# Kernel optimization log

Hardware: AMD Instinct MI355X
Metric: run time of the kernel (lower is better)

## Reference

```python
import jax, jax.numpy as jnp
import numpy as np

B, NPG, F, H, DEG = 2048, 50, 64, 2, 8  # graphs, nodes/graph, feat dim, heads, avg degree
N = B * NPG
NEG_SLOPE_ATTN = 0.2   # DGL GATConv default leaky slope
NEG_SLOPE_ACT = 0.1    # module's LeakyReLU


def setup_inputs() -> dict:
    key = jax.random.key(0)
    ks = jax.random.split(key, 24)
    node_feats = jax.random.normal(ks[0], (N, F), dtype=jnp.float32)
    # within-graph random edges + self loops (avoids zero in-degree)
    E = N * DEG
    base = jnp.repeat(jnp.arange(B, dtype=jnp.int32) * NPG, NPG * DEG)
    src = base + jax.random.randint(ks[1], (E,), 0, NPG, dtype=jnp.int32)
    dst = base + jax.random.randint(ks[2], (E,), 0, NPG, dtype=jnp.int32)
    loops = jnp.arange(N, dtype=jnp.int32)
    src = jnp.concatenate([src, loops])
    dst = jnp.concatenate([dst, loops])
    s = 0.1
    params = dict(
        W0=jax.random.normal(ks[3], (F, H * F)) * s,
        al0=jax.random.normal(ks[4], (H, F)) * s,
        ar0=jax.random.normal(ks[5], (H, F)) * s,
        resW0=jax.random.normal(ks[6], (F, H * F)) * s,
        g0=jnp.ones((H * F,)), b0=jnp.zeros((H * F,)),
        W1=jax.random.normal(ks[7], (H * F, H * F)) * s,
        al1=jax.random.normal(ks[8], (H, F)) * s,
        ar1=jax.random.normal(ks[9], (H, F)) * s,
        g1=jnp.ones((H * F,)), b1=jnp.zeros((H * F,)),
        W2=jax.random.normal(ks[10], (H * F, H * F)) * s,
        al2=jax.random.normal(ks[11], (H, F)) * s,
        ar2=jax.random.normal(ks[12], (H, F)) * s,
        g2=jnp.ones((H * F,)), b2=jnp.zeros((H * F,)),
    )
    return {"node_feats": node_feats, **params, "src": src, "dst": dst}


def _gat(h, src, dst, W, al, ar, resW):
    """DGL GATConv (bias=False, residual=True, no activation). resW=None -> identity residual."""
    feat = (h @ W).reshape(N, H, F)                      # [N,H,F]
    el = jnp.sum(feat * al, -1)                          # [N,H]
    er = jnp.sum(feat * ar, -1)
    e = jax.nn.leaky_relu(el[src] + er[dst], NEG_SLOPE_ATTN)  # [E,H]
    m = jax.ops.segment_max(e, dst, num_segments=N)
    ex = jnp.exp(e - m[dst])
    denom = jax.ops.segment_sum(ex, dst, num_segments=N)
    a = ex / denom[dst]                                  # edge softmax per dst node
    rst = jax.ops.segment_sum(a[:, :, None] * feat[src], dst, num_segments=N)
    res = (h @ resW) if resW is not None else h
    return rst + res.reshape(N, H, F)


def _norm(x, g, b):
    mu = jnp.mean(x, -1, keepdims=True)
    v = jnp.mean((x - mu) ** 2, -1, keepdims=True)
    return (x - mu) / jnp.sqrt(v + 1e-5) * g + b


def reference(node_feats, W0, al0, ar0, resW0, g0, b0,
              W1, al1, ar1, g1, b1, W2, al2, ar2, g2, b2, src, dst):
    graph_ids = jnp.arange(N) // NPG
    layers = [(W0, al0, ar0, resW0, g0, b0),
              (W1, al1, ar1, None, g1, b1),
              (W2, al2, ar2, None, g2, b2)]
    h = node_feats
    embeddings = []
    for (W, al, ar, resW, g, b) in layers:
        h = _gat(h, src, dst, W, al, ar, resW).reshape(N, H * F)  # flatten(1)
        h = _norm(h, g, b)
        h = jax.nn.leaky_relu(h, NEG_SLOPE_ACT)
        per_node = h.reshape(N, H, F).mean(1)                     # mean over heads
        emb = jax.ops.segment_sum(per_node, graph_ids, num_segments=B) / NPG  # mean_nodes
        embeddings.append(emb)
    out = jnp.concatenate(embeddings, axis=-1)                    # JK 'cat' -> [B, 3F]
    return jax.nn.leaky_relu(out, NEG_SLOPE_ACT)
```

## Files before the change

kernel.cpp:

```cpp
#include <hip/hip_runtime.h>

#define NPG    50
#define HF     128
#define FDIM   64
#define NGRAPH 2048
#define EPG    400
#define SP     72
#define HB     136
#define CNTW   16

typedef __attribute__((ext_vector_type(8))) short bf16x8;
typedef __attribute__((ext_vector_type(4))) float floatx4;
typedef __bf16 bfv2 __attribute__((ext_vector_type(2)));

__device__ __forceinline__ float leaky(float x, float s) { return x >= 0.f ? x : x * s; }

__device__ __forceinline__ unsigned short f2bf(float f) {
    __bf16 b = (__bf16)f;
    unsigned short u;
    __builtin_memcpy(&u, &b, 2);
    return u;
}
__device__ __forceinline__ unsigned f2bfpk(float a, float b) {
    bfv2 v;
    v[0] = (__bf16)a;
    v[1] = (__bf16)b;
    unsigned u;
    __builtin_memcpy(&u, &v, 4);
    return u;
}
__device__ __forceinline__ float bf2f(unsigned short h) {
    return __uint_as_float(((unsigned)h) << 16);
}
__device__ __forceinline__ int fkey(float f) { int b = __float_as_int(f); return b >= 0 ? b : b ^ 0x7fffffff; }
__device__ __forceinline__ float funkey(int k) { return __int_as_float(k >= 0 ? k : k ^ 0x7fffffff); }

template <int CTRL>
__device__ __forceinline__ float dpp_addx(float x) {
    int yi = __builtin_amdgcn_update_dpp(0, __float_as_int(x), CTRL, 0xf, 0xf, true);
    return x + __int_as_float(yi);
}
__device__ __forceinline__ float row16_sum(float x) {
    x = dpp_addx<0xB1>(x);
    x = dpp_addx<0x4E>(x);
    x = dpp_addx<0x141>(x);
    x = dpp_addx<0x140>(x);
    return x;
}


__global__ void prep_w(const float* __restrict__ W0, const float* __restrict__ rW0,
                       const float* __restrict__ W1, const float* __restrict__ W2,
                       const float* __restrict__ al0, const float* __restrict__ ar0,
                       const float* __restrict__ al1, const float* __restrict__ ar1,
                       const float* __restrict__ al2, const float* __restrict__ ar2,
                       unsigned short* __restrict__ wt0, unsigned short* __restrict__ wt1,
                       unsigned short* __restrict__ wt2) {
    if (blockIdx.x >= 64) {
        int gid = (blockIdx.x - 64) * 256 + threadIdx.x;
        if (gid < 1024) {
            int la = gid >> 6, k = gid & 63;
            unsigned short o = 0;
            if (la < 8) {
                const float* a = (la < 4) ? al0 : ar0;
                int h = (la >> 1) & 1;
                float v = 0.f;
                for (int f = 0; f < 64; ++f) v += W0[k * 128 + h * 64 + f] * a[h * 64 + f];
                __bf16 hi = (__bf16)v;
                if (la & 1) o = f2bf(v - (float)hi);
                else __builtin_memcpy(&o, &hi, 2);
            }
            wt0[(256 + la) * 64 + k] = o;
        } else {
            int q = gid - 1024;
            int l = q >> 11;
            int la = (q >> 7) & 15, kp = q & 127;
            int ktrue = (kp & 64) + ((kp & 3) * 16) + ((kp & 63) >> 2);
            const float* W = l ? W2 : W1;
            unsigned short o = 0;
            if (la < 8) {
                const float* a = l ? ((la < 4) ? al2 : ar2) : ((la < 4) ? al1 : ar1);
                int h = (la >> 1) & 1;
                float v = 0.f;
                for (int f = 0; f < 64; ++f) v += W[ktrue * 128 + h * 64 + f] * a[h * 64 + f];
                __bf16 hi = (__bf16)v;
                if (la & 1) o = f2bf(v - (float)hi);
                else __builtin_memcpy(&o, &hi, 2);
            }
            (l ? wt2 : wt1)[(128 + la) * 128 + kp] = o;
        }
        return;
    }
    int i = blockIdx.x * 256 + threadIdx.x;
    if (i < 256 * 64) {
        int n = i >> 6, k = i & 63;
        float v = (n < 128) ? W0[k * 128 + n] : rW0[k * 128 + (n - 128)];
        wt0[i] = f2bf(v);
    }
    if (i < 128 * 128) {
        int n = i >> 7, kp = i & 127;
        int ktrue = (kp & 64) + ((kp & 3) * 16) + ((kp & 63) >> 2);
        wt1[i] = f2bf(W1[ktrue * 128 + n]);
        wt2[i] = f2bf(W2[ktrue * 128 + n]);
    }
}

template <int K, bool RESW>
__device__ __forceinline__ void gat_layer(
    const float* __restrict__ xrow,
    const unsigned short* __restrict__ Wt,
    const float* __restrict__ gp, const float* __restrict__ bp,
    float* __restrict__ out, int layer, int g, int t,
    unsigned short* featT, unsigned short* hbuf, int* cnt,
    float* el_s, float* er_s, int* elmax_i,
    float* lnp, float* lnq, float* psum4, float* gbL)
{
    const int w = t >> 6, lane = t & 63, quad = lane >> 4, l16 = lane & 15;
    constexpr int KS = K / 32;
    constexpr int ATTN_ROW = RESW ? 256 : 128;
    const int mt = w & 3;
    int mrow = mt * 16 + l16;
    if (mrow >= NPG) mrow = NPG - 1;
    const floatx4 zf = {0.f, 0.f, 0.f, 0.f};

    if (t < HF) {
        int p = (t & 64) + ((t & 15) * 4) + ((t >> 4) & 3);
        gbL[p] = gp[t];
        gbL[HF + p] = bp[t];
    }

    bf16x8 afr[KS];
    if constexpr (RESW) {
        const float* hrow = xrow + (size_t)mrow * 64;
#pragma unroll
        for (int ks = 0; ks < KS; ++ks) {
            int k0 = ks * 32 + quad * 8;
            float4 p0 = *(const float4*)(hrow + k0);
            float4 p1 = *(const float4*)(hrow + k0 + 4);
            unsigned au[4] = {f2bfpk(p0.x, p0.y), f2bfpk(p0.z, p0.w),
                              f2bfpk(p1.x, p1.y), f2bfpk(p1.z, p1.w)};
            __builtin_memcpy(&afr[ks], au, 16);
        }
    } else {
#pragma unroll
        for (int ks = 0; ks < KS; ++ks)
            afr[ks] = *(const bf16x8*)&hbuf[mrow * HB + ks * 32 + quad * 8];
    }

    if constexpr (RESW) {
#pragma unroll 1
        for (int half = 0; half < 2; ++half) {
            const int nb = (w >> 2) * 8 + half * 4;
            floatx4 acc[4];
#pragma unroll
            for (int nt = 0; nt < 4; ++nt) acc[nt] = zf;
#pragma unroll
            for (int nt = 0; nt < 4; ++nt) {
                const unsigned short* wrow = Wt + (size_t)((nb + nt) * 16 + l16) * K;
#pragma unroll
                for (int ks = 0; ks < KS; ++ks) {
                    bf16x8 b = *(const bf16x8*)(wrow + ks * 32 + quad * 8);
                    acc[nt] = __builtin_amdgcn_mfma_f32_16x16x32_bf16(afr[ks], b, acc[nt], 0, 0, 0);
                }
            }
#pragma unroll
            for (int nt = 0; nt < 4; ++nt) {
                int n = (nb + nt) * 16 + l16;
                if (n < HF) {
                    uint2 pk = {f2bfpk(acc[nt][0], acc[nt][1]),
                                f2bfpk(acc[nt][2], acc[nt][3])};
                    *(uint2*)&featT[n * SP + mt * 16 + quad * 4] = pk;
                } else {
                    int c = n - HF;
                    int spos = (c & 64) + ((c & 15) * 4) + ((c >> 4) & 3);
#pragma unroll
                    for (int r = 0; r < 4; ++r) {
                        int dr = mt * 16 + quad * 4 + r;
                        if (dr < NPG) hbuf[dr * HB + spos] = f2bf(acc[nt][r]);
                    }
                }
            }
        }
    } else {
        const int ntbase = (w >> 2) * 4;
        floatx4 acc[4];
#pragma unroll
        for (int nt = 0; nt < 4; ++nt) acc[nt] = zf;
#pragma unroll
        for (int nt = 0; nt < 4; ++nt) {
            const unsigned short* wrow = Wt + (size_t)((ntbase + nt) * 16 + l16) * K;
#pragma unroll
            for (int ks = 0; ks < KS; ++ks) {
                bf16x8 b = *(const bf16x8*)(wrow + ks * 32 + quad * 8);
                acc[nt] = __builtin_amdgcn_mfma_f32_16x16x32_bf16(afr[ks], b, acc[nt], 0, 0, 0);
            }
        }
#pragma unroll
        for (int nt = 0; nt < 4; ++nt) {
            int n = (ntbase + nt) * 16 + l16;
            uint2 pk = {f2bfpk(acc[nt][0], acc[nt][1]),
                        f2bfpk(acc[nt][2], acc[nt][3])};
            *(uint2*)&featT[n * SP + mt * 16 + quad * 4] = pk;
        }
    }

    if (w < 4) {
        floatx4 ae = zf;
        const unsigned short* wrow = Wt + (size_t)(ATTN_ROW + l16) * K;
#pragma unroll
        for (int ks = 0; ks < KS; ++ks) {
            bf16x8 b = *(const bf16x8*)(wrow + ks * 32 + quad * 8);
            ae = __builtin_amdgcn_mfma_f32_16x16x32_bf16(afr[ks], b, ae, 0, 0, 0);
        }
#pragma unroll
        for (int r = 0; r < 4; ++r) {
            float v = dpp_addx<0xB1>(ae[r]);
            if ((l16 & 1) == 0 && l16 < 8) {
                int row = mt * 16 + quad * 4 + r;
                int hd2 = (l16 >> 1) & 1;
                if (l16 < 4) {
                    el_s[hd2 * 64 + row] = v;
                    atomicMax(&elmax_i[hd2], fkey(v));
                } else {
                    er_s[hd2 * 64 + row] = v;
                }
            }
        }
    }
    __syncthreads();

    const int hd = w >> 2, amt = w & 3;
    const int d = amt * 16 + l16;

    const float erd = er_s[hd * 64 + d];
    const float md = leaky(funkey(elmax_i[hd]) + erd, 0.2f);
    const int dcl = d < NPG ? d : NPG - 1;
    const int* crow = &cnt[dcl * CNTW];

    bf16x8 ap[2];
    float rowsum = 0.f;
#pragma unroll
    for (int ks = 0; ks < 2; ++ks) {
        float4 ev0 = *(const float4*)&el_s[hd * 64 + ks * 32 + quad * 8];
        float4 ev1 = *(const float4*)&el_s[hd * 64 + ks * 32 + quad * 8 + 4];
        const float ev[8] = {ev0.x, ev0.y, ev0.z, ev0.w, ev1.x, ev1.y, ev1.z, ev1.w};
        int2 cw = *(const int2*)&crow[ks * 8 + quad * 2];
        unsigned au[4];
#pragma unroll
        for (int jp = 0; jp < 4; ++jp) {
            float e0 = ev[2 * jp] + erd;
            float e1 = ev[2 * jp + 1] + erd;
            e0 = fmaxf(e0, 0.2f * e0);
            e1 = fmaxf(e1, 0.2f * e1);
            float p0 = __expf(e0 - md);
            float p1 = __expf(e1 - md);
            int w32 = (jp & 2) ? cw.y : cw.x;
            int sh = (jp & 1) * 16;
            int c0 = (w32 >> sh) & 0xff;
            int c1 = (w32 >> (sh + 8)) & 0xff;
            unsigned pk = f2bfpk((float)c0 * p0, (float)c1 * p1);
            au[jp] = pk;
            rowsum += __uint_as_float(pk << 16) + __uint_as_float(pk & 0xffff0000u);
        }
        __builtin_memcpy(&ap[ks], au, 16);
    }
    rowsum += __shfl_xor(rowsum, 16, 64);
    rowsum += __shfl_xor(rowsum, 32, 64);
    const float rden = 1.f / fmaxf(rowsum, 1e-30f);

    floatx4 ag[4];
#pragma unroll
    for (int nt = 0; nt < 4; ++nt) ag[nt] = zf;
#pragma unroll
    for (int nt = 0; nt < 4; ++nt) {
        const unsigned short* fr = &featT[(hd * 64 + nt * 16 + l16) * SP];
#pragma unroll
        for (int ks = 0; ks < 2; ++ks) {
            bf16x8 b = *(const bf16x8*)(fr + ks * 32 + quad * 8);
            ag[nt] = __builtin_amdgcn_mfma_f32_16x16x32_bf16(ap[ks], b, ag[nt], 0, 0, 0);
        }
    }

    float s1[4] = {0, 0, 0, 0}, s2[4] = {0, 0, 0, 0};
#pragma unroll
    for (int r = 0; r < 4; ++r) {
        int dd = amt * 16 + quad * 4 + r;
        int dc = dd < NPG ? dd : NPG - 1;
        float rdv = __shfl(rden, quad * 4 + r, 16);
        uint2 rv = *(const uint2*)&hbuf[dc * HB + hd * 64 + l16 * 4];
#pragma unroll
        for (int nt = 0; nt < 4; ++nt) {
            unsigned hw = (nt & 1) ? ((nt & 2) ? rv.y >> 16 : rv.x >> 16)
                                   : ((nt & 2) ? rv.y & 0xffffu : rv.x & 0xffffu);
            float vv = fmaf(ag[nt][r], rdv, bf2f((unsigned short)hw));
            ag[nt][r] = vv;
            s1[r] += vv;
            s2[r] = fmaf(vv, vv, s2[r]);
        }
    }
#pragma unroll
    for (int r = 0; r < 4; ++r) {
        s1[r] = row16_sum(s1[r]);
        s2[r] = row16_sum(s2[r]);
    }
    if (l16 == 0) {
#pragma unroll
        for (int r = 0; r < 4; ++r) {
            int dd = amt * 16 + quad * 4 + r;
            lnp[hd * 64 + dd] = s1[r];
            lnq[hd * 64 + dd] = s2[r];
        }
    }
    __syncthreads();

    if (t < 2) elmax_i[t] = (int)0x80000000;

    float4 ga = *(const float4*)&gbL[hd * 64 + l16 * 4];
    float4 ba = *(const float4*)&gbL[HF + hd * 64 + l16 * 4];

    float part[4] = {0, 0, 0, 0};
#pragma unroll
    for (int r = 0; r < 4; ++r) {
        int dd = amt * 16 + quad * 4 + r;
        if (dd < NPG) {
            float mu = (lnp[dd] + lnp[64 + dd]) * (1.f / HF);
            float rs = rsqrtf((lnq[dd] + lnq[64 + dd]) * (1.f / HF) - mu * mu + 1e-5f);
            float y4[4];
#pragma unroll
            for (int nt = 0; nt < 4; ++nt) {
                float y = (ag[nt][r] - mu) * rs * ga[nt] + ba[nt];
                y = leaky(y, 0.1f);
                y4[nt] = y;
                part[nt] += y;
            }
            uint2 pk = {f2bfpk(y4[0], y4[1]), f2bfpk(y4[2], y4[3])};
            *(uint2*)&hbuf[dd * HB + hd * 64 + l16 * 4] = pk;
        }
    }
#pragma unroll
    for (int nt = 0; nt < 4; ++nt) {
        part[nt] += __shfl_xor(part[nt], 16, 64);
        part[nt] += __shfl_xor(part[nt], 32, 64);
    }
    if (quad == 0) {
#pragma unroll
        for (int nt = 0; nt < 4; ++nt)
            psum4[amt * HF + hd * 64 + nt * 16 + l16] = part[nt];
    }
    __syncthreads();

    if (t < FDIM) {
        float s = 0.f;
#pragma unroll
        for (int a4 = 0; a4 < 4; ++a4)
            s += psum4[a4 * HF + t] + psum4[a4 * HF + t + FDIM];
        out[(size_t)g * (3 * FDIM) + layer * FDIM + t] = leaky(s * (1.f / (2 * NPG)), 0.1f);
    }
}

__global__ __launch_bounds__(512, 8) void gat3_kernel(
    const float* __restrict__ x,
    const unsigned short* __restrict__ wt0,
    const unsigned short* __restrict__ wt1,
    const unsigned short* __restrict__ wt2,
    const float* __restrict__ g0, const float* __restrict__ b0,
    const float* __restrict__ g1, const float* __restrict__ b1,
    const float* __restrict__ g2, const float* __restrict__ b2,
    const int* __restrict__ src, const int* __restrict__ dst,
    float* __restrict__ out)
{
    __shared__ unsigned short featT[HF * SP];
    __shared__ unsigned short hbuf[NPG * HB];
    __shared__ int cnt[NPG * CNTW];
    __shared__ float el_s[128], er_s[128];
    __shared__ int elmax_i[2];
    __shared__ float lnp[128], lnq[128];
    __shared__ float psum4[4 * HF];
    __shared__ float gbL[2 * HF];

    const int g = blockIdx.x, t = threadIdx.x;
    const int nbase = g * NPG;

    int es = 0, ed = 0;
    if (t < EPG) { es = src[g * EPG + t] - nbase; ed = dst[g * EPG + t] - nbase; }

    for (int i = t; i < NPG * CNTW; i += 512) cnt[i] = 0;
    if (t < 2) elmax_i[t] = (int)0x80000000;
    __syncthreads();

    if (t < EPG) atomicAdd(&cnt[ed * CNTW + (es >> 2)], 1 << ((es & 3) * 8));
    if (t < NPG) atomicAdd(&cnt[t * CNTW + (t >> 2)], 1 << ((t & 3) * 8));

    const float* xrow = x + (size_t)nbase * 64;
    gat_layer<64, true>(xrow, wt0, g0, b0, out, 0, g, t,
                        featT, hbuf, cnt, el_s, er_s, elmax_i, lnp, lnq, psum4, gbL);
    gat_layer<128, false>(nullptr, wt1, g1, b1, out, 1, g, t,
                          featT, hbuf, cnt, el_s, er_s, elmax_i, lnp, lnq, psum4, gbL);
    gat_layer<128, false>(nullptr, wt2, g2, b2, out, 2, g, t,
                          featT, hbuf, cnt, el_s, er_s, elmax_i, lnp, lnq, psum4, gbL);
}

extern "C" void kernel_launch(void* const* d_in, const int* in_sizes, int n_in,
                              void* d_out, int out_size, void* d_ws, size_t ws_size,
                              hipStream_t stream) {
    const float* x   = (const float*)d_in[0];
    const float* W0  = (const float*)d_in[1];
    const float* al0 = (const float*)d_in[2];
    const float* ar0 = (const float*)d_in[3];
    const float* rW0 = (const float*)d_in[4];
    const float* g0  = (const float*)d_in[5];
    const float* b0  = (const float*)d_in[6];
    const float* W1  = (const float*)d_in[7];
    const float* al1 = (const float*)d_in[8];
    const float* ar1 = (const float*)d_in[9];
    const float* g1  = (const float*)d_in[10];
    const float* b1  = (const float*)d_in[11];
    const float* W2  = (const float*)d_in[12];
    const float* al2 = (const float*)d_in[13];
    const float* ar2 = (const float*)d_in[14];
    const float* g2  = (const float*)d_in[15];
    const float* b2  = (const float*)d_in[16];
    const int* src   = (const int*)d_in[17];
    const int* dst   = (const int*)d_in[18];
    float* out = (float*)d_out;

    unsigned short* wt0 = (unsigned short*)d_ws;
    unsigned short* wt1 = wt0 + 272 * 64;
    unsigned short* wt2 = wt1 + 144 * 128;

    prep_w<<<84, 256, 0, stream>>>(W0, rW0, W1, W2, al0, ar0, al1, ar1, al2, ar2,
                                   wt0, wt1, wt2);
    gat3_kernel<<<NGRAPH, 512, 0, stream>>>(
        x, wt0, wt1, wt2, g0, b0, g1, b1, g2, b2, src, dst, out);
}
```

Measured before the change: 227.7 us.

## Cut register pressure by streaming A-fragments and recomputing aggregation MFMAs

The GEMM loops now keep K-slices rolled and load the A-fragment per k-step from LDS in the non-residual layers, instead of holding all afr[KS] in registers. The aggregation MFMA results are no longer kept live across the layernorm barrier. They are recomputed in two passes of two column tiles, one pass for the statistics and one for the normalize and write. This lowers VGPR usage to allow higher occupancy, at the cost of doubled aggregation MFMAs, extra LDS reads, and less instruction-level parallelism from the rolled loops.

```diff
diff --git a/kernel.cpp b/kernel.cpp
--- a/kernel.cpp
+++ b/kernel.cpp
@@ -129,37 +129,31 @@
         gbL[HF + p] = bp[t];
     }
 
-    bf16x8 afr[KS];
     if constexpr (RESW) {
-        const float* hrow = xrow + (size_t)mrow * 64;
-#pragma unroll
-        for (int ks = 0; ks < KS; ++ks) {
-            int k0 = ks * 32 + quad * 8;
-            float4 p0 = *(const float4*)(hrow + k0);
-            float4 p1 = *(const float4*)(hrow + k0 + 4);
-            unsigned au[4] = {f2bfpk(p0.x, p0.y), f2bfpk(p0.z, p0.w),
-                              f2bfpk(p1.x, p1.y), f2bfpk(p1.z, p1.w)};
-            __builtin_memcpy(&afr[ks], au, 16);
-        }
-    } else {
-#pragma unroll
-        for (int ks = 0; ks < KS; ++ks)
-            afr[ks] = *(const bf16x8*)&hbuf[mrow * HB + ks * 32 + quad * 8];
-    }
-
-    if constexpr (RESW) {
+        bf16x8 afr[KS];
+        {
+            const float* hrow = xrow + (size_t)mrow * 64;
+#pragma unroll
+            for (int ks = 0; ks < KS; ++ks) {
+                int k0 = ks * 32 + quad * 8;
+                float4 p0 = *(const float4*)(hrow + k0);
+                float4 p1 = *(const float4*)(hrow + k0 + 4);
+                unsigned au[4] = {f2bfpk(p0.x, p0.y), f2bfpk(p0.z, p0.w),
+                                  f2bfpk(p1.x, p1.y), f2bfpk(p1.z, p1.w)};
+                __builtin_memcpy(&afr[ks], au, 16);
+            }
+        }
 #pragma unroll 1
         for (int half = 0; half < 2; ++half) {
             const int nb = (w >> 2) * 8 + half * 4;
             floatx4 acc[4];
 #pragma unroll
             for (int nt = 0; nt < 4; ++nt) acc[nt] = zf;
-#pragma unroll
-            for (int nt = 0; nt < 4; ++nt) {
-                const unsigned short* wrow = Wt + (size_t)((nb + nt) * 16 + l16) * K;
-#pragma unroll
-                for (int ks = 0; ks < KS; ++ks) {
-                    bf16x8 b = *(const bf16x8*)(wrow + ks * 32 + quad * 8);
+#pragma unroll 1
+            for (int ks = 0; ks < KS; ++ks) {
+#pragma unroll
+                for (int nt = 0; nt < 4; ++nt) {
+                    bf16x8 b = *(const bf16x8*)(Wt + (size_t)((nb + nt) * 16 + l16) * K + ks * 32 + quad * 8);
                     acc[nt] = __builtin_amdgcn_mfma_f32_16x16x32_bf16(afr[ks], b, acc[nt], 0, 0, 0);
                 }
             }
@@ -181,18 +175,41 @@
                 }
             }
         }
+        if (w < 4) {
+            floatx4 ae = zf;
+            const unsigned short* wrow = Wt + (size_t)(ATTN_ROW + l16) * K;
+#pragma unroll
+            for (int ks = 0; ks < KS; ++ks) {
+                bf16x8 b = *(const bf16x8*)(wrow + ks * 32 + quad * 8);
+                ae = __builtin_amdgcn_mfma_f32_16x16x32_bf16(afr[ks], b, ae, 0, 0, 0);
+            }
+#pragma unroll
+            for (int r = 0; r < 4; ++r) {
+                float v = dpp_addx<0xB1>(ae[r]);
+                if ((l16 & 1) == 0 && l16 < 8) {
+                    int row = mt * 16 + quad * 4 + r;
+                    int hd2 = (l16 >> 1) & 1;
+                    if (l16 < 4) {
+                        el_s[hd2 * 64 + row] = v;
+                        atomicMax(&elmax_i[hd2], fkey(v));
+                    } else {
+                        er_s[hd2 * 64 + row] = v;
+                    }
+                }
+            }
+        }
     } else {
         const int ntbase = (w >> 2) * 4;
         floatx4 acc[4];
 #pragma unroll
         for (int nt = 0; nt < 4; ++nt) acc[nt] = zf;
-#pragma unroll
-        for (int nt = 0; nt < 4; ++nt) {
-            const unsigned short* wrow = Wt + (size_t)((ntbase + nt) * 16 + l16) * K;
-#pragma unroll
-            for (int ks = 0; ks < KS; ++ks) {
-                bf16x8 b = *(const bf16x8*)(wrow + ks * 32 + quad * 8);
-                acc[nt] = __builtin_amdgcn_mfma_f32_16x16x32_bf16(afr[ks], b, acc[nt], 0, 0, 0);
+#pragma unroll 1
+        for (int ks = 0; ks < KS; ++ks) {
+            bf16x8 a = *(const bf16x8*)&hbuf[mrow * HB + ks * 32 + quad * 8];
+#pragma unroll
+            for (int nt = 0; nt < 4; ++nt) {
+                bf16x8 b = *(const bf16x8*)(Wt + (size_t)((ntbase + nt) * 16 + l16) * K + ks * 32 + quad * 8);
+                acc[nt] = __builtin_amdgcn_mfma_f32_16x16x32_bf16(a, b, acc[nt], 0, 0, 0);
             }
         }
 #pragma unroll
@@ -202,27 +219,26 @@
                         f2bfpk(acc[nt][2], acc[nt][3])};
             *(uint2*)&featT[n * SP + mt * 16 + quad * 4] = pk;
         }
-    }
-
-    if (w < 4) {
-        floatx4 ae = zf;
-        const unsigned short* wrow = Wt + (size_t)(ATTN_ROW + l16) * K;
-#pragma unroll
-        for (int ks = 0; ks < KS; ++ks) {
-            bf16x8 b = *(const bf16x8*)(wrow + ks * 32 + quad * 8);
-            ae = __builtin_amdgcn_mfma_f32_16x16x32_bf16(afr[ks], b, ae, 0, 0, 0);
-        }
-#pragma unroll
-        for (int r = 0; r < 4; ++r) {
-            float v = dpp_addx<0xB1>(ae[r]);
-            if ((l16 & 1) == 0 && l16 < 8) {
-                int row = mt * 16 + quad * 4 + r;
-                int hd2 = (l16 >> 1) & 1;
-                if (l16 < 4) {
-                    el_s[hd2 * 64 + row] = v;
-                    atomicMax(&elmax_i[hd2], fkey(v));
-                } else {
-                    er_s[hd2 * 64 + row] = v;
+        if (w < 4) {
+            floatx4 ae = zf;
+#pragma unroll 1
+            for (int ks = 0; ks < KS; ++ks) {
+                bf16x8 a = *(const bf16x8*)&hbuf[mrow * HB + ks * 32 + quad * 8];
+                bf16x8 b = *(const bf16x8*)(Wt + (size_t)(ATTN_ROW + l16) * K + ks * 32 + quad * 8);
+                ae = __builtin_amdgcn_mfma_f32_16x16x32_bf16(a, b, ae, 0, 0, 0);
+            }
+#pragma unroll
+            for (int r = 0; r < 4; ++r) {
+                float v = dpp_addx<0xB1>(ae[r]);
+                if ((l16 & 1) == 0 && l16 < 8) {
+                    int row = mt * 16 + quad * 4 + r;
+                    int hd2 = (l16 >> 1) & 1;
+                    if (l16 < 4) {
+                        el_s[hd2 * 64 + row] = v;
+                        atomicMax(&elmax_i[hd2], fkey(v));
+                    } else {
+                        er_s[hd2 * 64 + row] = v;
+                    }
                 }
             }
         }
@@ -268,34 +284,31 @@
     rowsum += __shfl_xor(rowsum, 32, 64);
     const float rden = 1.f / fmaxf(rowsum, 1e-30f);
 
-    floatx4 ag[4];
-#pragma unroll
-    for (int nt = 0; nt < 4; ++nt) ag[nt] = zf;
-#pragma unroll
-    for (int nt = 0; nt < 4; ++nt) {
-        const unsigned short* fr = &featT[(hd * 64 + nt * 16 + l16) * SP];
+    float s1[4] = {0, 0, 0, 0}, s2[4] = {0, 0, 0, 0};
+#pragma unroll 1
+    for (int ntp = 0; ntp < 2; ++ntp) {
+        floatx4 ag2[2] = {zf, zf};
 #pragma unroll
         for (int ks = 0; ks < 2; ++ks) {
-            bf16x8 b = *(const bf16x8*)(fr + ks * 32 + quad * 8);
-            ag[nt] = __builtin_amdgcn_mfma_f32_16x16x32_bf16(ap[ks], b, ag[nt], 0, 0, 0);
-        }
-    }
-
-    float s1[4] = {0, 0, 0, 0}, s2[4] = {0, 0, 0, 0};
-#pragma unroll
-    for (int r = 0; r < 4; ++r) {
-        int dd = amt * 16 + quad * 4 + r;
-        int dc = dd < NPG ? dd : NPG - 1;
-        float rdv = __shfl(rden, quad * 4 + r, 16);
-        uint2 rv = *(const uint2*)&hbuf[dc * HB + hd * 64 + l16 * 4];
-#pragma unroll
-        for (int nt = 0; nt < 4; ++nt) {
-            unsigned hw = (nt & 1) ? ((nt & 2) ? rv.y >> 16 : rv.x >> 16)
-                                   : ((nt & 2) ? rv.y & 0xffffu : rv.x & 0xffffu);
-            float vv = fmaf(ag[nt][r], rdv, bf2f((unsigned short)hw));
-            ag[nt][r] = vv;
-            s1[r] += vv;
-            s2[r] = fmaf(vv, vv, s2[r]);
+#pragma unroll
+            for (int ntn = 0; ntn < 2; ++ntn) {
+                int nt = ntp * 2 + ntn;
+                bf16x8 b = *(const bf16x8*)&featT[(hd * 64 + nt * 16 + l16) * SP + ks * 32 + quad * 8];
+                ag2[ntn] = __builtin_amdgcn_mfma_f32_16x16x32_bf16(ap[ks], b, ag2[ntn], 0, 0, 0);
+            }
+        }
+#pragma unroll
+        for (int r = 0; r < 4; ++r) {
+            int dd = amt * 16 + quad * 4 + r;
+            int dc = dd < NPG ? dd : NPG - 1;
+            float rdv = __shfl(rden, quad * 4 + r, 16);
+            unsigned rv = *(const unsigned*)&hbuf[dc * HB + hd * 64 + l16 * 4 + ntp * 2];
+            float vv0 = fmaf(ag2[0][r], rdv, bf2f((unsigned short)(rv & 0xffffu)));
+            float vv1 = fmaf(ag2[1][r], rdv, bf2f((unsigned short)(rv >> 16)));
+            s1[r] += vv0;
+            s1[r] += vv1;
+            s2[r] = fmaf(vv0, vv0, s2[r]);
+            s2[r] = fmaf(vv1, vv1, s2[r]);
         }
     }
 #pragma unroll
@@ -315,26 +328,37 @@
 
     if (t < 2) elmax_i[t] = (int)0x80000000;
 
-    float4 ga = *(const float4*)&gbL[hd * 64 + l16 * 4];
-    float4 ba = *(const float4*)&gbL[HF + hd * 64 + l16 * 4];
-
     float part[4] = {0, 0, 0, 0};
-#pragma unroll
-    for (int r = 0; r < 4; ++r) {
-        int dd = amt * 16 + quad * 4 + r;
-        if (dd < NPG) {
-            float mu = (lnp[dd] + lnp[64 + dd]) * (1.f / HF);
-            float rs = rsqrtf((lnq[dd] + lnq[64 + dd]) * (1.f / HF) - mu * mu + 1e-5f);
-            float y4[4];
-#pragma unroll
-            for (int nt = 0; nt < 4; ++nt) {
-                float y = (ag[nt][r] - mu) * rs * ga[nt] + ba[nt];
-                y = leaky(y, 0.1f);
-                y4[nt] = y;
-                part[nt] += y;
-            }
-            uint2 pk = {f2bfpk(y4[0], y4[1]), f2bfpk(y4[2], y4[3])};
-            *(uint2*)&hbuf[dd * HB + hd * 64 + l16 * 4] = pk;
+#pragma unroll 1
+    for (int ntp = 0; ntp < 2; ++ntp) {
+        floatx4 ag2[2] = {zf, zf};
+#pragma unroll
+        for (int ks = 0; ks < 2; ++ks) {
+#pragma unroll
+            for (int ntn = 0; ntn < 2; ++ntn) {
+                int nt = ntp * 2 + ntn;
+                bf16x8 b = *(const bf16x8*)&featT[(hd * 64 + nt * 16 + l16) * SP + ks * 32 + quad * 8];
+                ag2[ntn] = __builtin_amdgcn_mfma_f32_16x16x32_bf16(ap[ks], b, ag2[ntn], 0, 0, 0);
+            }
+        }
+        float2 ga2 = *(const float2*)&gbL[hd * 64 + l16 * 4 + ntp * 2];
+        float2 ba2 = *(const float2*)&gbL[HF + hd * 64 + l16 * 4 + ntp * 2];
+#pragma unroll
+        for (int r = 0; r < 4; ++r) {
+            int dd = amt * 16 + quad * 4 + r;
+            float rdv = __shfl(rden, quad * 4 + r, 16);
+            if (dd < NPG) {
+                unsigned rv = *(const unsigned*)&hbuf[dd * HB + hd * 64 + l16 * 4 + ntp * 2];
+                float vv0 = fmaf(ag2[0][r], rdv, bf2f((unsigned short)(rv & 0xffffu)));
+                float vv1 = fmaf(ag2[1][r], rdv, bf2f((unsigned short)(rv >> 16)));
+                float mu = (lnp[dd] + lnp[64 + dd]) * (1.f / HF);
+                float rs = rsqrtf((lnq[dd] + lnq[64 + dd]) * (1.f / HF) - mu * mu + 1e-5f);
+                float y0 = leaky((vv0 - mu) * rs * ga2.x + ba2.x, 0.1f);
+                float y1 = leaky((vv1 - mu) * rs * ga2.y + ba2.y, 0.1f);
+                part[ntp * 2]     += y0;
+                part[ntp * 2 + 1] += y1;
+                *(unsigned*)&hbuf[dd * HB + hd * 64 + l16 * 4 + ntp * 2] = f2bfpk(y0, y1);
+            }
         }
     }
 #pragma unroll
```

New measurement: 273.4 us. +20.1%, slower.

## Double threads per graph block, splitting GEMM and aggregation column tiles across waves

Applied to the files above, without the earlier changes.

Raises the block size from 512 to 1024 threads (16 waves) per graph. Each wave now computes half as many output column tiles in the projection GEMM and in the attention aggregation, and LayerNorm partial sums are kept per wave half and combined. The aim is more latency hiding and less serial MFMA work per wave, at the cost of fewer blocks resident per CU, a register budget tightened by the 1024-thread launch bound, and redundant softmax-weight computation in both wave halves.

```diff
diff --git a/kernel.cpp b/kernel.cpp
--- a/kernel.cpp
+++ b/kernel.cpp
@@ -8,6 +8,7 @@
 #define SP     72
 #define HB     136
 #define CNTW   16
+#define NTHR   1024
 
 typedef __attribute__((ext_vector_type(8))) short bf16x8;
 typedef __attribute__((ext_vector_type(4))) float floatx4;
@@ -119,6 +120,7 @@
     constexpr int KS = K / 32;
     constexpr int ATTN_ROW = RESW ? 256 : 128;
     const int mt = w & 3;
+    const int ng = w >> 2;
     int mrow = mt * 16 + l16;
     if (mrow >= NPG) mrow = NPG - 1;
     const floatx4 zf = {0.f, 0.f, 0.f, 0.f};
@@ -150,12 +152,10 @@
     if constexpr (RESW) {
 #pragma unroll 1
         for (int half = 0; half < 2; ++half) {
-            const int nb = (w >> 2) * 8 + half * 4;
-            floatx4 acc[4];
-#pragma unroll
-            for (int nt = 0; nt < 4; ++nt) acc[nt] = zf;
-#pragma unroll
-            for (int nt = 0; nt < 4; ++nt) {
+            const int nb = ng * 4 + half * 2;
+            floatx4 acc[2] = {zf, zf};
+#pragma unroll
+            for (int nt = 0; nt < 2; ++nt) {
                 const unsigned short* wrow = Wt + (size_t)((nb + nt) * 16 + l16) * K;
 #pragma unroll
                 for (int ks = 0; ks < KS; ++ks) {
@@ -164,7 +164,7 @@
                 }
             }
 #pragma unroll
-            for (int nt = 0; nt < 4; ++nt) {
+            for (int nt = 0; nt < 2; ++nt) {
                 int n = (nb + nt) * 16 + l16;
                 if (n < HF) {
                     uint2 pk = {f2bfpk(acc[nt][0], acc[nt][1]),
@@ -182,12 +182,10 @@
             }
         }
     } else {
-        const int ntbase = (w >> 2) * 4;
-        floatx4 acc[4];
-#pragma unroll
-        for (int nt = 0; nt < 4; ++nt) acc[nt] = zf;
-#pragma unroll
-        for (int nt = 0; nt < 4; ++nt) {
+        const int ntbase = ng * 2;
+        floatx4 acc[2] = {zf, zf};
+#pragma unroll
+        for (int nt = 0; nt < 2; ++nt) {
             const unsigned short* wrow = Wt + (size_t)((ntbase + nt) * 16 + l16) * K;
 #pragma unroll
             for (int ks = 0; ks < KS; ++ks) {
@@ -196,7 +194,7 @@
             }
         }
 #pragma unroll
-        for (int nt = 0; nt < 4; ++nt) {
+        for (int nt = 0; nt < 2; ++nt) {
             int n = (ntbase + nt) * 16 + l16;
             uint2 pk = {f2bfpk(acc[nt][0], acc[nt][1]),
                         f2bfpk(acc[nt][2], acc[nt][3])};
@@ -229,7 +227,7 @@
     }
     __syncthreads();
 
-    const int hd = w >> 2, amt = w & 3;
+    const int hd = w >> 3, amt = (w >> 1) & 3, ntp = w & 1;
     const int d = amt * 16 + l16;
 
     const float erd = er_s[hd * 64 + d];
@@ -268,16 +266,14 @@
     rowsum += __shfl_xor(rowsum, 32, 64);
     const float rden = 1.f / fmaxf(rowsum, 1e-30f);
 
-    floatx4 ag[4];
-#pragma unroll
-    for (int nt = 0; nt < 4; ++nt) ag[nt] = zf;
-#pragma unroll
-    for (int nt = 0; nt < 4; ++nt) {
-        const unsigned short* fr = &featT[(hd * 64 + nt * 16 + l16) * SP];
-#pragma unroll
-        for (int ks = 0; ks < 2; ++ks) {
-            bf16x8 b = *(const bf16x8*)(fr + ks * 32 + quad * 8);
-            ag[nt] = __builtin_amdgcn_mfma_f32_16x16x32_bf16(ap[ks], b, ag[nt], 0, 0, 0);
+    floatx4 ag2[2] = {zf, zf};
+#pragma unroll
+    for (int ks = 0; ks < 2; ++ks) {
+#pragma unroll
+        for (int ntn = 0; ntn < 2; ++ntn) {
+            int nt = ntp * 2 + ntn;
+            bf16x8 b = *(const bf16x8*)&featT[(hd * 64 + nt * 16 + l16) * SP + ks * 32 + quad * 8];
+            ag2[ntn] = __builtin_amdgcn_mfma_f32_16x16x32_bf16(ap[ks], b, ag2[ntn], 0, 0, 0);
         }
     }
 
@@ -287,16 +283,15 @@
         int dd = amt * 16 + quad * 4 + r;
         int dc = dd < NPG ? dd : NPG - 1;
         float rdv = __shfl(rden, quad * 4 + r, 16);
-        uint2 rv = *(const uint2*)&hbuf[dc * HB + hd * 64 + l16 * 4];
-#pragma unroll
-        for (int nt = 0; nt < 4; ++nt) {
-            unsigned hw = (nt & 1) ? ((nt & 2) ? rv.y >> 16 : rv.x >> 16)
-                                   : ((nt & 2) ? rv.y & 0xffffu : rv.x & 0xffffu);
-            float vv = fmaf(ag[nt][r], rdv, bf2f((unsigned short)hw));
-            ag[nt][r] = vv;
-            s1[r] += vv;
-            s2[r] = fmaf(vv, vv, s2[r]);
-        }
+        unsigned rv = *(const unsigned*)&hbuf[dc * HB + hd * 64 + l16 * 4 + ntp * 2];
+        float vv0 = fmaf(ag2[0][r], rdv, bf2f((unsigned short)(rv & 0xffffu)));
+        float vv1 = fmaf(ag2[1][r], rdv, bf2f((unsigned short)(rv >> 16)));
+        ag2[0][r] = vv0;
+        ag2[1][r] = vv1;
+        s1[r] += vv0;
+        s1[r] += vv1;
+        s2[r] = fmaf(vv0, vv0, s2[r]);
+        s2[r] = fmaf(vv1, vv1, s2[r]);
     }
 #pragma unroll
     for (int r = 0; r < 4; ++r) {
@@ -307,45 +302,42 @@
 #pragma unroll
         for (int r = 0; r < 4; ++r) {
             int dd = amt * 16 + quad * 4 + r;
-            lnp[hd * 64 + dd] = s1[r];
-            lnq[hd * 64 + dd] = s2[r];
+            lnp[ntp * 128 + hd * 64 + dd] = s1[r];
+            lnq[ntp * 128 + hd * 64 + dd] = s2[r];
         }
     }
     __syncthreads();
 
     if (t < 2) elmax_i[t] = (int)0x80000000;
 
-    float4 ga = *(const float4*)&gbL[hd * 64 + l16 * 4];
-    float4 ba = *(const float4*)&gbL[HF + hd * 64 + l16 * 4];
-
-    float part[4] = {0, 0, 0, 0};
+    float2 ga2 = *(const float2*)&gbL[hd * 64 + l16 * 4 + ntp * 2];
+    float2 ba2 = *(const float2*)&gbL[HF + hd * 64 + l16 * 4 + ntp * 2];
+
+    float part[2] = {0, 0};
 #pragma unroll
     for (int r = 0; r < 4; ++r) {
         int dd = amt * 16 + quad * 4 + r;
         if (dd < NPG) {
-            float mu = (lnp[dd] + lnp[64 + dd]) * (1.f / HF);
-            float rs = rsqrtf((lnq[dd] + lnq[64 + dd]) * (1.f / HF) - mu * mu + 1e-5f);
-            float y4[4];
-#pragma unroll
-            for (int nt = 0; nt < 4; ++nt) {
-                float y = (ag[nt][r] - mu) * rs * ga[nt] + ba[nt];
-                y = leaky(y, 0.1f);
-                y4[nt] = y;
-                part[nt] += y;
-            }
-            uint2 pk = {f2bfpk(y4[0], y4[1]), f2bfpk(y4[2], y4[3])};
-            *(uint2*)&hbuf[dd * HB + hd * 64 + l16 * 4] = pk;
-        }
-    }
-#pragma unroll
-    for (int nt = 0; nt < 4; ++nt) {
-        part[nt] += __shfl_xor(part[nt], 16, 64);
-        part[nt] += __shfl_xor(part[nt], 32, 64);
+            float mus = (lnp[dd] + lnp[64 + dd]) + (lnp[128 + dd] + lnp[192 + dd]);
+            float sqs = (lnq[dd] + lnq[64 + dd]) + (lnq[128 + dd] + lnq[192 + dd]);
+            float mu = mus * (1.f / HF);
+            float rs = rsqrtf(sqs * (1.f / HF) - mu * mu + 1e-5f);
+            float y0 = leaky((ag2[0][r] - mu) * rs * ga2.x + ba2.x, 0.1f);
+            float y1 = leaky((ag2[1][r] - mu) * rs * ga2.y + ba2.y, 0.1f);
+            part[0] += y0;
+            part[1] += y1;
+            *(unsigned*)&hbuf[dd * HB + hd * 64 + l16 * 4 + ntp * 2] = f2bfpk(y0, y1);
+        }
+    }
+#pragma unroll
+    for (int j = 0; j < 2; ++j) {
+        part[j] += __shfl_xor(part[j], 16, 64);
+        part[j] += __shfl_xor(part[j], 32, 64);
     }
     if (quad == 0) {
 #pragma unroll
-        for (int nt = 0; nt < 4; ++nt)
-            psum4[amt * HF + hd * 64 + nt * 16 + l16] = part[nt];
+        for (int j = 0; j < 2; ++j)
+            psum4[amt * HF + hd * 64 + (ntp * 2 + j) * 16 + l16] = part[j];
     }
     __syncthreads();
 
@@ -358,7 +350,7 @@
     }
 }
 
-__global__ __launch_bounds__(512, 8) void gat3_kernel(
+__global__ __launch_bounds__(NTHR, 8) void gat3_kernel(
     const float* __restrict__ x,
     const unsigned short* __restrict__ wt0,
     const unsigned short* __restrict__ wt1,
@@ -374,7 +366,7 @@
     __shared__ int cnt[NPG * CNTW];
     __shared__ float el_s[128], er_s[128];
     __shared__ int elmax_i[2];
-    __shared__ float lnp[128], lnq[128];
+    __shared__ float lnp[256], lnq[256];
     __shared__ float psum4[4 * HF];
     __shared__ float gbL[2 * HF];
 
@@ -384,7 +376,7 @@
     int es = 0, ed = 0;
     if (t < EPG) { es = src[g * EPG + t] - nbase; ed = dst[g * EPG + t] - nbase; }
 
-    for (int i = t; i < NPG * CNTW; i += 512) cnt[i] = 0;
+    for (int i = t; i < NPG * CNTW; i += NTHR) cnt[i] = 0;
     if (t < 2) elmax_i[t] = (int)0x80000000;
     __syncthreads();
 
@@ -430,6 +422,6 @@
 
     prep_w<<<84, 256, 0, stream>>>(W0, rW0, W1, W2, al0, ar0, al1, ar1, al2, ar2,
                                    wt0, wt1, wt2);
-    gat3_kernel<<<NGRAPH, 512, 0, stream>>>(
+    gat3_kernel<<<NGRAPH, NTHR, 0, stream>>>(
         x, wt0, wt1, wt2, g0, b0, g1, b1, g2, b2, src, dst, out);
 }
```

After: 294.9 us. 1.3x slower.

## Stage GAT weights into LDS via async DMA, prefetching next layer's weights

Applied to the files above, without the earlier changes.

Each layer's bf16 weight matrix is now copied into a shared-memory buffer with global_load_lds DMA and an XOR swizzle, and the MFMA B-operands are read from LDS instead of straight from global memory. The next layer's weights are fetched right after the projection barrier, so the copy runs alongside the attention, aggregation and norm phases of the current layer. This aims to remove repeated per-wave global and L2 weight loads from the matmul critical path. In exchange each block uses about 36 KB more LDS and the launch-bounds occupancy hint drops from 8 to 4, which cuts blocks per CU and may hurt latency hiding.

```diff
diff --git a/kernel.cpp b/kernel.cpp
--- a/kernel.cpp
+++ b/kernel.cpp
@@ -34,6 +34,29 @@
 }
 __device__ __forceinline__ int fkey(float f) { int b = __float_as_int(f); return b >= 0 ? b : b ^ 0x7fffffff; }
 __device__ __forceinline__ float funkey(int k) { return __int_as_float(k >= 0 ? k : k ^ 0x7fffffff); }
+
+__device__ __forceinline__ void gld16(const void* g, void* l) {
+    __builtin_amdgcn_global_load_lds(
+        (const __attribute__((address_space(1))) void*)g,
+        (__attribute__((address_space(3))) void*)l, 16, 0, 0);
+}
+
+__device__ __forceinline__ void stage_wt(const unsigned short* __restrict__ wg,
+                                         unsigned short* wtbuf, int t,
+                                         int totb, int krsh) {
+    const int w = t >> 6, lane = t & 63;
+    for (int c = w; c * 1024 < totb; c += 8) {
+        int G = c * 1024 + lane * 16;
+        int Gs = G ^ (((G >> krsh) & 7) << 4);
+        gld16((const char*)wg + Gs, (char*)wtbuf + c * 1024);
+    }
+}
+
+template <int KROWB>
+__device__ __forceinline__ bf16x8 wt_read(const unsigned short* wtbuf, int row, int cb) {
+    int byte = (row * KROWB + cb) ^ ((row & 7) << 4);
+    return *(const bf16x8*)((const char*)wtbuf + byte);
+}
 
 template <int CTRL>
 __device__ __forceinline__ float dpp_addx(float x) {
@@ -105,18 +128,19 @@
     }
 }
 
-template <int K, bool RESW>
+template <int K, bool RESW, bool STAGE_NEXT>
 __device__ __forceinline__ void gat_layer(
     const float* __restrict__ xrow,
-    const unsigned short* __restrict__ Wt,
+    const unsigned short* __restrict__ wnext,
     const float* __restrict__ gp, const float* __restrict__ bp,
     float* __restrict__ out, int layer, int g, int t,
-    unsigned short* featT, unsigned short* hbuf, int* cnt,
+    unsigned short* wtbuf, unsigned short* featT, unsigned short* hbuf, int* cnt,
     float* el_s, float* er_s, int* elmax_i,
     float* lnp, float* lnq, float* psum4, float* gbL)
 {
     const int w = t >> 6, lane = t & 63, quad = lane >> 4, l16 = lane & 15;
     constexpr int KS = K / 32;
+    constexpr int KROWB = 2 * K;
     constexpr int ATTN_ROW = RESW ? 256 : 128;
     const int mt = w & 3;
     int mrow = mt * 16 + l16;
@@ -156,10 +180,9 @@
             for (int nt = 0; nt < 4; ++nt) acc[nt] = zf;
 #pragma unroll
             for (int nt = 0; nt < 4; ++nt) {
-                const unsigned short* wrow = Wt + (size_t)((nb + nt) * 16 + l16) * K;
 #pragma unroll
                 for (int ks = 0; ks < KS; ++ks) {
-                    bf16x8 b = *(const bf16x8*)(wrow + ks * 32 + quad * 8);
+                    bf16x8 b = wt_read<KROWB>(wtbuf, (nb + nt) * 16 + l16, ks * 64 + quad * 16);
                     acc[nt] = __builtin_amdgcn_mfma_f32_16x16x32_bf16(afr[ks], b, acc[nt], 0, 0, 0);
                 }
             }
@@ -188,10 +211,9 @@
         for (int nt = 0; nt < 4; ++nt) acc[nt] = zf;
 #pragma unroll
         for (int nt = 0; nt < 4; ++nt) {
-            const unsigned short* wrow = Wt + (size_t)((ntbase + nt) * 16 + l16) * K;
 #pragma unroll
             for (int ks = 0; ks < KS; ++ks) {
-                bf16x8 b = *(const bf16x8*)(wrow + ks * 32 + quad * 8);
+                bf16x8 b = wt_read<KROWB>(wtbuf, (ntbase + nt) * 16 + l16, ks * 64 + quad * 16);
                 acc[nt] = __builtin_amdgcn_mfma_f32_16x16x32_bf16(afr[ks], b, acc[nt], 0, 0, 0);
             }
         }
@@ -206,10 +228,9 @@
 
     if (w < 4) {
         floatx4 ae = zf;
-        const unsigned short* wrow = Wt + (size_t)(ATTN_ROW + l16) * K;
 #pragma unroll
         for (int ks = 0; ks < KS; ++ks) {
-            bf16x8 b = *(const bf16x8*)(wrow + ks * 32 + quad * 8);
+            bf16x8 b = wt_read<KROWB>(wtbuf, ATTN_ROW + l16, ks * 64 + quad * 16);
             ae = __builtin_amdgcn_mfma_f32_16x16x32_bf16(afr[ks], b, ae, 0, 0, 0);
         }
 #pragma unroll
@@ -228,6 +249,8 @@
         }
     }
     __syncthreads();
+
+    if constexpr (STAGE_NEXT) stage_wt(wnext, wtbuf, t, 144 * 256, 8);
 
     const int hd = w >> 2, amt = w & 3;
     const int d = amt * 16 + l16;
@@ -358,7 +381,7 @@
     }
 }
 
-__global__ __launch_bounds__(512, 8) void gat3_kernel(
+__global__ __launch_bounds__(512, 4) void gat3_kernel(
     const float* __restrict__ x,
     const unsigned short* __restrict__ wt0,
     const unsigned short* __restrict__ wt1,
@@ -369,6 +392,7 @@
     const int* __restrict__ src, const int* __restrict__ dst,
     float* __restrict__ out)
 {
+    __shared__ unsigned short wtbuf[144 * 128];
     __shared__ unsigned short featT[HF * SP];
     __shared__ unsigned short hbuf[NPG * HB];
     __shared__ int cnt[NPG * CNTW];
@@ -381,6 +405,8 @@
     const int g = blockIdx.x, t = threadIdx.x;
     const int nbase = g * NPG;
 
+    stage_wt(wt0, wtbuf, t, 272 * 128, 7);
+
     int es = 0, ed = 0;
     if (t < EPG) { es = src[g * EPG + t] - nbase; ed = dst[g * EPG + t] - nbase; }
 
@@ -392,12 +418,12 @@
     if (t < NPG) atomicAdd(&cnt[t * CNTW + (t >> 2)], 1 << ((t & 3) * 8));
 
     const float* xrow = x + (size_t)nbase * 64;
-    gat_layer<64, true>(xrow, wt0, g0, b0, out, 0, g, t,
-                        featT, hbuf, cnt, el_s, er_s, elmax_i, lnp, lnq, psum4, gbL);
-    gat_layer<128, false>(nullptr, wt1, g1, b1, out, 1, g, t,
-                          featT, hbuf, cnt, el_s, er_s, elmax_i, lnp, lnq, psum4, gbL);
-    gat_layer<128, false>(nullptr, wt2, g2, b2, out, 2, g, t,
-                          featT, hbuf, cnt, el_s, er_s, elmax_i, lnp, lnq, psum4, gbL);
+    gat_layer<64, true, true>(xrow, wt1, g0, b0, out, 0, g, t,
+                              wtbuf, featT, hbuf, cnt, el_s, er_s, elmax_i, lnp, lnq, psum4, gbL);
+    gat_layer<128, false, true>(nullptr, wt2, g1, b1, out, 1, g, t,
+                                wtbuf, featT, hbuf, cnt, el_s, er_s, elmax_i, lnp, lnq, psum4, gbL);
+    gat_layer<128, false, false>(nullptr, nullptr, g2, b2, out, 2, g, t,
+                                 wtbuf, featT, hbuf, cnt, el_s, er_s, elmax_i, lnp, lnq, psum4, gbL);
 }
 
 extern "C" void kernel_launch(void* const* d_in, const int* in_sizes, int n_in,
```

Measured after the change: 182.9 us. -19.7%, faster.
